# Optimization experiments

Measured on AMD Instinct MI355X. Metric: run time of the kernel, lower is better.

Reference implementation:

```python
import jax, jax.numpy as jnp
import numpy as np

N, E = 20000, 320000
IN, OUT, MID, EC, L = 128, 128, 32, 32, 1
SQRT3 = 1.7320508075688772
EPS = 1e-5


def _xavier(key, fan_in, fan_out, shape=None):
    shape = shape if shape is not None else (fan_in, fan_out)
    std = (2.0 / (fan_in + fan_out)) ** 0.5
    return jax.random.normal(key, shape, dtype=jnp.float32) * std


def layer_norm(x, w, b):
    mu = x.mean(axis=-1, keepdims=True)
    var = ((x - mu) ** 2).mean(axis=-1, keepdims=True)
    return (x - mu) * jax.lax.rsqrt(var + EPS) * w + b


def equ_layer_norm(x, w, b, lmax):
    # x: [N, (lmax+1)^2, C]; per-l RMS norm over (m, channel); l=0 mean-centered + bias.
    segs = []
    for l in range(lmax + 1):
        f = x[:, l * l:(l + 1) * (l + 1), :]
        if l == 0:
            f = f - f.mean(axis=-1, keepdims=True)
        norm = jnp.mean(f * f, axis=(1, 2), keepdims=True)
        f = f * jax.lax.rsqrt(norm + EPS) * w[l]
        if l == 0:
            f = f + b
        segs.append(f)
    return jnp.concatenate(segs, axis=1)


def gate_3j(x, w, lmax, channel):
    # x: [N, (lmax+1)^2, C]; w: [C, C*(lmax+1)] (jax in,out layout)
    after = x[:, 0, :] @ w
    type0 = after[:, :channel]
    mult = jax.nn.sigmoid(after[:, channel:])  # [N, lmax*C]
    parts = [jax.nn.silu(type0)[:, None, :]]
    for l in range(1, lmax + 1):
        parts.append(x[:, l * l:(l + 1) * (l + 1), :] * mult[:, None, (l - 1) * channel:l * channel])
    return jnp.concatenate(parts, axis=1)


def setup_inputs() -> dict:
    key = jax.random.key(0)
    ks = jax.random.split(key, 24)
    inp = {
        'feats': jax.random.normal(ks[0], (N, IN), dtype=jnp.float32),
        'equ': jax.random.normal(ks[1], (N, (L + 1) ** 2, EC), dtype=jnp.float32),
        'points': jax.random.normal(ks[2], (N, 3), dtype=jnp.float32),
        'neighbors': jax.random.randint(ks[3], (2, E), 0, N, dtype=jnp.int64) if jax.config.jax_enable_x64 else jax.random.randint(ks[3], (2, E), 0, N, dtype=jnp.int32),
        # params (jax Linear layout: [in, out])
        'ln1_w': jnp.ones((IN,), jnp.float32), 'ln1_b': jnp.zeros((IN,), jnp.float32),
        'eqn1_w': jnp.ones((L + 1, EC), jnp.float32), 'eqn1_b': jnp.zeros((EC,), jnp.float32),
        'inv_fc_w': _xavier(ks[4], IN, MID), 'inv_fc_b': jnp.zeros((MID,), jnp.float32),
        'equ_fc_w': _xavier(ks[5], EC, MID),
        'fc_l0_w': _xavier(ks[6], 2 * MID, MID), 'fc_l0_b': jnp.zeros((MID,), jnp.float32),
        'equ_fc_2_w': _xavier(ks[7], MID, EC),
        'inv_fc_1_w': _xavier(ks[8], 3 * MID, OUT), 'inv_fc_1_b': jnp.zeros((OUT,), jnp.float32),
        'ffn_ln_w': jnp.ones((OUT,), jnp.float32), 'ffn_ln_b': jnp.zeros((OUT,), jnp.float32),
        'ffn_w1': _xavier(ks[9], OUT, OUT), 'ffn_b1': jnp.zeros((OUT,), jnp.float32),
        'ffn_w2': _xavier(ks[10], OUT, OUT), 'ffn_b2': jnp.zeros((OUT,), jnp.float32),
        'eqn2_w': jnp.ones((L + 1, EC), jnp.float32), 'eqn2_b': jnp.zeros((EC,), jnp.float32),
        'fe1_w': _xavier(ks[11], EC, MID),
        'gate_w': _xavier(ks[12], MID, MID * (L + 1)),
        'fe2_w': _xavier(ks[13], MID, EC),
    }
    return inp


def reference(feats, equ, points, neighbors, ln1_w, ln1_b, eqn1_w, eqn1_b,
              inv_fc_w, inv_fc_b, equ_fc_w, fc_l0_w, fc_l0_b, equ_fc_2_w,
              inv_fc_1_w, inv_fc_1_b, ffn_ln_w, ffn_ln_b, ffn_w1, ffn_b1,
              ffn_w2, ffn_b2, eqn2_w, eqn2_b, fe1_w, gate_w, fe2_w):
    n = feats.shape[0]
    feats = layer_norm(feats, ln1_w, ln1_b)
    equ = equ_layer_norm(equ, eqn1_w, eqn1_b, L)
    feats1 = feats @ inv_fc_w + inv_fc_b              # [N, MID]
    equ1 = equ @ equ_fc_w                              # [N, 4, MID]
    src, dst = neighbors[0], neighbors[1]
    s_equ, t_equ = equ1[src], equ1[dst]                # [E, 4, MID]
    s_feats, t_feats = feats1[src], feats1[dst]        # [E, MID]
    vec = points[src] - points[dst]                    # [E, 3]
    # e3nn spherical harmonics l=0..1, normalize=False, 'component': [1, sqrt(3)*v]
    sh = jnp.concatenate([jnp.ones((vec.shape[0], 1), vec.dtype), SQRT3 * vec], axis=1)  # [E, 4]
    dot1 = jnp.sum(s_equ * t_equ, axis=1)              # [E, MID]
    dot2 = jnp.sum(s_equ * sh[:, :, None], axis=1)     # [E, MID]
    equ_l0 = jax.nn.silu(jnp.concatenate([dot1, dot2], axis=1) @ fc_l0_w + fc_l0_b)
    equ_message = jnp.concatenate([equ_l0[:, None, :], s_equ[:, 1:, :]], axis=1)  # [E, 4, MID]
    equ_message = equ_message @ equ_fc_2_w             # [E, 4, EC]
    inv_message = jax.nn.silu(jnp.concatenate([s_feats, t_feats, equ_l0], axis=-1) @ inv_fc_1_w + inv_fc_1_b)  # [E, OUT]
    nb_cnt = (jnp.max(inv_message, axis=-1, keepdims=True) > 0.0).astype(feats.dtype)  # [E, 1]
    neighbors_new = jnp.ones((n, 1), feats.dtype).at[dst].add(nb_cnt)
    inv_new = jnp.zeros((n, OUT), feats.dtype).at[dst].add(inv_message) + feats  # shortcut1 = Identity
    inv_new = inv_new / neighbors_new
    equ_new = jnp.zeros((n, (L + 1) ** 2, EC), feats.dtype).at[dst].add(equ_message) + equ  # shortcut2 = Identity
    equ_new = equ_new / neighbors_new[:, :, None]
    # ffn_inv
    h = layer_norm(inv_new, ffn_ln_w, ffn_ln_b)
    h = jax.nn.relu(h @ ffn_w1 + ffn_b1) @ ffn_w2 + ffn_b2
    inv_new = h + inv_new
    # ffn_equ
    g = equ_layer_norm(equ_new, eqn2_w, eqn2_b, L) @ fe1_w
    g = gate_3j(g, gate_w, L, MID) @ fe2_w
    equ_new = g + equ_new
    return inv_new, equ_new
```

## Files before the change

kernel.cpp:

```cpp
#include <hip/hip_runtime.h>
#include <math.h>

#define EPS 1e-5f
#define SQRT3F 1.7320508075688772f

__device__ __forceinline__ float wsum64(float x) {
#pragma unroll
    for (int o = 32; o > 0; o >>= 1) x += __shfl_xor(x, o, 64);
    return x;
}
__device__ __forceinline__ float hsum32(float x) {
#pragma unroll
    for (int o = 16; o > 0; o >>= 1) x += __shfl_xor(x, o, 64);
    return x;
}
__device__ __forceinline__ float sigm(float x) { return 1.f / (1.f + __expf(-x)); }
__device__ __forceinline__ float siluf(float x) { return x * sigm(x); }

__global__ __launch_bounds__(256) void node_pre(
    int N,
    const float* __restrict__ feats, const float* __restrict__ equ,
    const float* __restrict__ ln1_w, const float* __restrict__ ln1_b,
    const float* __restrict__ eqn1_w, const float* __restrict__ eqn1_b,
    const float* __restrict__ inv_fc_w, const float* __restrict__ inv_fc_b,
    const float* __restrict__ equ_fc_w, const float* __restrict__ Winv,
    float* __restrict__ feats_ln, float* __restrict__ equ_ln,
    float* __restrict__ equ1t, float* __restrict__ PsP, float* __restrict__ PtP)
{
    __shared__ float fl_s[4][128];
    __shared__ float el_s[4][128];
    __shared__ float f1_s[4][32];
    const int w = threadIdx.x >> 6;
    const int lane = threadIdx.x & 63;
    const int n = blockIdx.x * 4 + w;
    const bool act = n < N;
    const int c = lane & 31;
    const int half = lane >> 5;

    float x0 = 0.f, x1 = 0.f;
    if (act) { x0 = feats[n * 128 + lane]; x1 = feats[n * 128 + 64 + lane]; }
    float s  = wsum64(x0 + x1);
    float sq = wsum64(x0 * x0 + x1 * x1);
    float mu = s * (1.f / 128.f);
    float var = sq * (1.f / 128.f) - mu * mu;
    float rs = rsqrtf(var + EPS);
    float y0 = (x0 - mu) * rs * ln1_w[lane] + ln1_b[lane];
    float y1 = (x1 - mu) * rs * ln1_w[64 + lane] + ln1_b[64 + lane];
    if (act) { feats_ln[n * 128 + lane] = y0; feats_ln[n * 128 + 64 + lane] = y1; }
    fl_s[w][lane] = y0; fl_s[w][64 + lane] = y1;

    float a = 0.f, b = 0.f;
    if (act) { a = equ[n * 128 + lane]; b = equ[n * 128 + 64 + lane]; }
    float a0 = (half == 0) ? a : 0.f;
    float m0 = wsum64(a0) * (1.f / 32.f);
    float f0 = a0 - m0;
    float n0 = wsum64((half == 0) ? f0 * f0 : 0.f) * (1.f / 32.f);
    float rs0 = rsqrtf(n0 + EPS);
    float sq1 = ((half == 1) ? a * a : 0.f) + b * b;
    float n1 = wsum64(sq1) * (1.f / 96.f);
    float rs1 = rsqrtf(n1 + EPS);
    float w1c = eqn1_w[32 + c];
    float ea = (half == 0) ? (f0 * rs0 * eqn1_w[c] + eqn1_b[c]) : (a * rs1 * w1c);
    float eb = b * rs1 * w1c;
    if (act) { equ_ln[n * 128 + lane] = ea; equ_ln[n * 128 + 64 + lane] = eb; }
    el_s[w][lane] = ea; el_s[w][64 + lane] = eb;

    __syncthreads();

    {
        float acc = 0.f;
#pragma unroll 8
        for (int k = 0; k < 64; k++) {
            int kk = half * 64 + k;
            acc += fl_s[w][kk] * inv_fc_w[kk * 32 + c];
        }
        acc += __shfl_xor(acc, 32);
        if (half == 0) f1_s[w][c] = acc + inv_fc_b[c];
    }
    if (act) {
        float acc = 0.f, acc2 = 0.f;
#pragma unroll 8
        for (int k = 0; k < 32; k++) {
            float wv = equ_fc_w[k * 32 + c];
            acc  += el_s[w][half * 32 + k] * wv;
            acc2 += el_s[w][(half + 2) * 32 + k] * wv;
        }
        equ1t[n * 128 + c * 4 + half]     = acc;
        equ1t[n * 128 + c * 4 + half + 2] = acc2;
    }
    __syncthreads();
    if (!act) return;

    {
        const int jj = c;
        float4 aPs = {0.f, 0.f, 0.f, 0.f};
        float4 aPt = {0.f, 0.f, 0.f, 0.f};
#pragma unroll 4
        for (int k = 0; k < 16; k++) {
            int kk = half * 16 + k;
            float x = f1_s[w][kk];
            float4 w4 = *(const float4*)&Winv[kk * 128 + jj * 4];
            float4 v4 = *(const float4*)&Winv[(32 + kk) * 128 + jj * 4];
            aPs.x += x * w4.x; aPs.y += x * w4.y; aPs.z += x * w4.z; aPs.w += x * w4.w;
            aPt.x += x * v4.x; aPt.y += x * v4.y; aPt.z += x * v4.z; aPt.w += x * v4.w;
        }
        aPs.x += __shfl_xor(aPs.x, 32); aPs.y += __shfl_xor(aPs.y, 32);
        aPs.z += __shfl_xor(aPs.z, 32); aPs.w += __shfl_xor(aPs.w, 32);
        aPt.x += __shfl_xor(aPt.x, 32); aPt.y += __shfl_xor(aPt.y, 32);
        aPt.z += __shfl_xor(aPt.z, 32); aPt.w += __shfl_xor(aPt.w, 32);
        if (half == 0) {
            const float* ps = (const float*)&aPs;
            const float* pt = (const float*)&aPt;
#pragma unroll
            for (int i = 0; i < 4; i++) {
                int m = jj * 4 + i;
                PsP[n * 128 + (m & 31) * 4 + (m >> 5)] = ps[i];
                PtP[n * 128 + (m & 31) * 4 + (m >> 5)] = pt[i];
            }
        }
    }
}

__global__ __launch_bounds__(256) void csr_hist(int E, const int* __restrict__ nb,
                                                int* __restrict__ deg)
{
    int i = blockIdx.x * 256 + threadIdx.x;
    if (i < E) atomicAdd(&deg[nb[E + i]], 1);
}

__global__ __launch_bounds__(1024) void csr_scan(int N, const int* __restrict__ deg,
                                                 int* __restrict__ row_start,
                                                 int* __restrict__ cursor)
{
    __shared__ int part[1024];
    const int t = threadIdx.x;
    const int per = (N + 1023) / 1024;
    const int base = t * per;
    int s = 0;
    for (int i = 0; i < per; i++) { int idx = base + i; if (idx < N) s += deg[idx]; }
    part[t] = s;
    __syncthreads();
    for (int off = 1; off < 1024; off <<= 1) {
        int v = (t >= off) ? part[t - off] : 0;
        __syncthreads();
        part[t] += v;
        __syncthreads();
    }
    int run = (t > 0) ? part[t - 1] : 0;
    for (int i = 0; i < per; i++) {
        int idx = base + i;
        if (idx < N) { row_start[idx] = run; cursor[idx] = run; run += deg[idx]; }
    }
}

__global__ __launch_bounds__(256) void csr_scatter(int E, const int* __restrict__ nb,
                                                   int* __restrict__ cursor,
                                                   int* __restrict__ csr_src)
{
    int i = blockIdx.x * 256 + threadIdx.x;
    if (i < E) {
        int d = nb[E + i];
        int s = nb[i];
        int pos = atomicAdd(&cursor[d], 1);
        csr_src[pos] = s;
    }
}

__global__ __launch_bounds__(256) void edge_agg(
    int N,
    const int* __restrict__ row_start, const int* __restrict__ deg_arr,
    const int* __restrict__ csr_src,
    const float* __restrict__ points, const float* __restrict__ equ1t,
    const float* __restrict__ PsP, const float* __restrict__ PtP,
    const float* __restrict__ feats_ln, const float* __restrict__ equ_ln,
    const float* __restrict__ Wl0g, const float* __restrict__ bl0g,
    const float* __restrict__ We2g, const float* __restrict__ Winvg,
    const float* __restrict__ binvg,
    float* __restrict__ out_inv, float* __restrict__ out_equ)
{
    __shared__ float WeP[32 * 128];
    __shared__ float Wl0P[16 * 128];
    __shared__ float We2P[8 * 128];
    __shared__ float BinvP[128];
    __shared__ float bl0s[32];
    __shared__ float scr[8][128];

    for (int idx = threadIdx.x; idx < 4096; idx += 256) {
        int k = idx >> 7, r = idx & 127, cc = r >> 2, j = r & 3;
        WeP[idx] = Winvg[(64 + k) * 128 + j * 32 + cc];
    }
    for (int idx = threadIdx.x; idx < 2048; idx += 256) {
        int g = idx >> 7, r = idx & 127, cc = r >> 2, i = r & 3;
        Wl0P[idx] = Wl0g[(g * 4 + i) * 32 + cc];
    }
    for (int idx = threadIdx.x; idx < 1024; idx += 256) {
        int g = idx >> 7, r = idx & 127, cc = r >> 2, i = r & 3;
        We2P[idx] = We2g[(g * 4 + i) * 32 + cc];
    }
    if (threadIdx.x < 128) BinvP[threadIdx.x] = binvg[(threadIdx.x & 3) * 32 + (threadIdx.x >> 2)];
    if (threadIdx.x < 32) bl0s[threadIdx.x] = bl0g[threadIdx.x];
    __syncthreads();

    const int grp = threadIdx.x >> 5;
    const int c = threadIdx.x & 31;
    const int halfsel = grp & 1;
    const int n = blockIdx.x * 8 + grp;
    if (n >= N) return;

    const int start = row_start[n];
    const int len = deg_arr[n];
    float4 te4 = *(const float4*)&equ1t[n * 128 + c * 4];
    float4 pt4 = *(const float4*)&PtP[n * 128 + c * 4];
    const float pdx = points[n * 3 + 0], pdy = points[n * 3 + 1], pdz = points[n * 3 + 2];
    float4 base = *(const float4*)&BinvP[c * 4];
    base.x += pt4.x; base.y += pt4.y; base.z += pt4.z; base.w += pt4.w;

    float4 acc = {0.f, 0.f, 0.f, 0.f};
    float4 aer = {0.f, 0.f, 0.f, 0.f};
    int cnt = 0;
    int i = 0;

    for (; i + 2 <= len; i += 2) {
        const int s0 = csr_src[start + i];
        const int s1 = csr_src[start + i + 1];
        float4 a0 = *(const float4*)&equ1t[s0 * 128 + c * 4];
        float4 a1 = *(const float4*)&equ1t[s1 * 128 + c * 4];
        float4 p0 = *(const float4*)&PsP[s0 * 128 + c * 4];
        float4 p1 = *(const float4*)&PsP[s1 * 128 + c * 4];
        float dx0 = SQRT3F * (points[s0 * 3 + 0] - pdx);
        float dy0 = SQRT3F * (points[s0 * 3 + 1] - pdy);
        float dz0 = SQRT3F * (points[s0 * 3 + 2] - pdz);
        float dx1 = SQRT3F * (points[s1 * 3 + 0] - pdx);
        float dy1 = SQRT3F * (points[s1 * 3 + 1] - pdy);
        float dz1 = SQRT3F * (points[s1 * 3 + 2] - pdz);
        scr[grp][c]      = a0.x * te4.x + a0.y * te4.y + a0.z * te4.z + a0.w * te4.w;
        scr[grp][32 + c] = a0.x + a0.y * dx0 + a0.z * dy0 + a0.w * dz0;
        scr[grp][64 + c] = a1.x * te4.x + a1.y * te4.y + a1.z * te4.z + a1.w * te4.w;
        scr[grp][96 + c] = a1.x + a1.y * dx1 + a1.z * dy1 + a1.w * dz1;

        float e0acc = bl0s[c], e1acc = bl0s[c];
#pragma unroll
        for (int g = 0; g < 16; g++) {
            float4 w4 = *(const float4*)&Wl0P[g * 128 + c * 4];
            float4 d0 = *(const float4*)&scr[grp][g * 4];
            float4 d1 = *(const float4*)&scr[grp][64 + g * 4];
            e0acc += d0.x * w4.x + d0.y * w4.y + d0.z * w4.z + d0.w * w4.w;
            e1acc += d1.x * w4.x + d1.y * w4.y + d1.z * w4.z + d1.w * w4.w;
        }
        float el0_0 = siluf(e0acc);
        float el0_1 = siluf(e1acc);
        aer.x += el0_0 + el0_1;
        aer.y += a0.y + a1.y; aer.z += a0.z + a1.z; aer.w += a0.w + a1.w;
        scr[grp][c] = el0_0;
        scr[grp][32 + c] = el0_1;

        float4 m0 = base, m1 = base;
        m0.x += p0.x; m0.y += p0.y; m0.z += p0.z; m0.w += p0.w;
        m1.x += p1.x; m1.y += p1.y; m1.z += p1.z; m1.w += p1.w;
#pragma unroll
        for (int g = 0; g < 8; g++) {
            float4 x0 = *(const float4*)&scr[grp][g * 4];
            float4 x1 = *(const float4*)&scr[grp][32 + g * 4];
            const float* xp0 = (const float*)&x0;
            const float* xp1 = (const float*)&x1;
#pragma unroll
            for (int t = 0; t < 4; t++) {
                float4 w4 = *(const float4*)&WeP[(g * 4 + t) * 128 + c * 4];
                float v0 = xp0[t], v1 = xp1[t];
                m0.x += v0 * w4.x; m0.y += v0 * w4.y; m0.z += v0 * w4.z; m0.w += v0 * w4.w;
                m1.x += v1 * w4.x; m1.y += v1 * w4.y; m1.z += v1 * w4.z; m1.w += v1 * w4.w;
            }
        }
        m0.x = siluf(m0.x); m0.y = siluf(m0.y); m0.z = siluf(m0.z); m0.w = siluf(m0.w);
        m1.x = siluf(m1.x); m1.y = siluf(m1.y); m1.z = siluf(m1.z); m1.w = siluf(m1.w);
        acc.x += m0.x + m1.x; acc.y += m0.y + m1.y;
        acc.z += m0.z + m1.z; acc.w += m0.w + m1.w;
        float mx0 = fmaxf(fmaxf(m0.x, m0.y), fmaxf(m0.z, m0.w));
        float mx1 = fmaxf(fmaxf(m1.x, m1.y), fmaxf(m1.z, m1.w));
        unsigned long long b0 = __ballot(mx0 > 0.f);
        unsigned long long b1 = __ballot(mx1 > 0.f);
        cnt += ((unsigned int)(b0 >> (halfsel * 32)) != 0u);
        cnt += ((unsigned int)(b1 >> (halfsel * 32)) != 0u);
    }
    for (; i < len; i++) {
        const int s0 = csr_src[start + i];
        float4 a0 = *(const float4*)&equ1t[s0 * 128 + c * 4];
        float4 p0 = *(const float4*)&PsP[s0 * 128 + c * 4];
        float dx0 = SQRT3F * (points[s0 * 3 + 0] - pdx);
        float dy0 = SQRT3F * (points[s0 * 3 + 1] - pdy);
        float dz0 = SQRT3F * (points[s0 * 3 + 2] - pdz);
        scr[grp][c]      = a0.x * te4.x + a0.y * te4.y + a0.z * te4.z + a0.w * te4.w;
        scr[grp][32 + c] = a0.x + a0.y * dx0 + a0.z * dy0 + a0.w * dz0;
        float e0acc = bl0s[c];
#pragma unroll
        for (int g = 0; g < 16; g++) {
            float4 w4 = *(const float4*)&Wl0P[g * 128 + c * 4];
            float4 d0 = *(const float4*)&scr[grp][g * 4];
            e0acc += d0.x * w4.x + d0.y * w4.y + d0.z * w4.z + d0.w * w4.w;
        }
        float el0_0 = siluf(e0acc);
        aer.x += el0_0; aer.y += a0.y; aer.z += a0.z; aer.w += a0.w;
        scr[grp][c] = el0_0;
        float4 m0 = base;
        m0.x += p0.x; m0.y += p0.y; m0.z += p0.z; m0.w += p0.w;
#pragma unroll
        for (int g = 0; g < 8; g++) {
            float4 x0 = *(const float4*)&scr[grp][g * 4];
            const float* xp0 = (const float*)&x0;
#pragma unroll
            for (int t = 0; t < 4; t++) {
                float4 w4 = *(const float4*)&WeP[(g * 4 + t) * 128 + c * 4];
                float v0 = xp0[t];
                m0.x += v0 * w4.x; m0.y += v0 * w4.y; m0.z += v0 * w4.z; m0.w += v0 * w4.w;
            }
        }
        m0.x = siluf(m0.x); m0.y = siluf(m0.y); m0.z = siluf(m0.z); m0.w = siluf(m0.w);
        acc.x += m0.x; acc.y += m0.y; acc.z += m0.z; acc.w += m0.w;
        float mx0 = fmaxf(fmaxf(m0.x, m0.y), fmaxf(m0.z, m0.w));
        unsigned long long b0 = __ballot(mx0 > 0.f);
        cnt += ((unsigned int)(b0 >> (halfsel * 32)) != 0u);
    }

    const float inv_nbn = 1.f / (1.f + (float)cnt);
    out_inv[n * 128 + c]      = (acc.x + feats_ln[n * 128 + c])      * inv_nbn;
    out_inv[n * 128 + 32 + c] = (acc.y + feats_ln[n * 128 + 32 + c]) * inv_nbn;
    out_inv[n * 128 + 64 + c] = (acc.z + feats_ln[n * 128 + 64 + c]) * inv_nbn;
    out_inv[n * 128 + 96 + c] = (acc.w + feats_ln[n * 128 + 96 + c]) * inv_nbn;

    *(float4*)&scr[grp][c * 4] = aer;
    float4 eo = {0.f, 0.f, 0.f, 0.f};
#pragma unroll
    for (int g = 0; g < 8; g++) {
        float4 w4 = *(const float4*)&We2P[g * 128 + c * 4];
        const float* wp = (const float*)&w4;
#pragma unroll
        for (int t = 0; t < 4; t++) {
            float4 a4 = *(const float4*)&scr[grp][(g * 4 + t) * 4];
            float wv = wp[t];
            eo.x += a4.x * wv; eo.y += a4.y * wv; eo.z += a4.z * wv; eo.w += a4.w * wv;
        }
    }
    out_equ[n * 128 + c]      = (eo.x + equ_ln[n * 128 + c])      * inv_nbn;
    out_equ[n * 128 + 32 + c] = (eo.y + equ_ln[n * 128 + 32 + c]) * inv_nbn;
    out_equ[n * 128 + 64 + c] = (eo.z + equ_ln[n * 128 + 64 + c]) * inv_nbn;
    out_equ[n * 128 + 96 + c] = (eo.w + equ_ln[n * 128 + 96 + c]) * inv_nbn;
}

__global__ __launch_bounds__(256) void node_post(
    int N,
    const float* __restrict__ ffn_ln_w, const float* __restrict__ ffn_ln_b,
    const float* __restrict__ W1g, const float* __restrict__ b1g,
    const float* __restrict__ W2g, const float* __restrict__ b2g,
    const float* __restrict__ eqn2_w, const float* __restrict__ eqn2_b,
    const float* __restrict__ fe1, const float* __restrict__ gate_w,
    const float* __restrict__ fe2,
    float* __restrict__ io_inv, float* __restrict__ io_equ)
{
    __shared__ float ht[128 * 36];
    __shared__ float es[8][128];
    __shared__ float gs[8][128];
    __shared__ float fe1P[8 * 128];
    __shared__ float fe2P[8 * 128];
    __shared__ float gatePa[8 * 128];
    __shared__ float gatePb[8 * 128];

    for (int idx = threadIdx.x; idx < 1024; idx += 256) {
        int g = idx >> 7, r = idx & 127, cc = r >> 2, i = r & 3;
        fe1P[idx]   = fe1[(g * 4 + i) * 32 + cc];
        fe2P[idx]   = fe2[(g * 4 + i) * 32 + cc];
        gatePa[idx] = gate_w[(g * 4 + i) * 64 + cc];
        gatePb[idx] = gate_w[(g * 4 + i) * 64 + 32 + cc];
    }
    __syncthreads();

    const int grp = threadIdx.x >> 5;
    const int c = threadIdx.x & 31;

    for (int q = 0; q < 4; q++) {
        const int nd = grp * 4 + q;
        const int n = blockIdx.x * 32 + nd;
        if (n >= N) break;

        float eq0 = io_equ[n * 128 + c];
        float eq1 = io_equ[n * 128 + 32 + c];
        float eq2 = io_equ[n * 128 + 64 + c];
        float eq3 = io_equ[n * 128 + 96 + c];
        float m0 = hsum32(eq0) * (1.f / 32.f);
        float f0 = eq0 - m0;
        float n0 = hsum32(f0 * f0) * (1.f / 32.f);
        float rs0 = rsqrtf(n0 + EPS);
        float n1 = hsum32(eq1 * eq1 + eq2 * eq2 + eq3 * eq3) * (1.f / 96.f);
        float rs1 = rsqrtf(n1 + EPS);
        float w1c = eqn2_w[32 + c];
        float4 ev;
        ev.x = f0 * rs0 * eqn2_w[c] + eqn2_b[c];
        ev.y = eq1 * rs1 * w1c;
        ev.z = eq2 * rs1 * w1c;
        ev.w = eq3 * rs1 * w1c;
        *(float4*)&es[grp][c * 4] = ev;

        float4 g4 = {0.f, 0.f, 0.f, 0.f};
#pragma unroll
        for (int g = 0; g < 8; g++) {
            float4 w4 = *(const float4*)&fe1P[g * 128 + c * 4];
            const float* wp = (const float*)&w4;
#pragma unroll
            for (int t = 0; t < 4; t++) {
                float4 a4 = *(const float4*)&es[grp][(g * 4 + t) * 4];
                float wv = wp[t];
                g4.x += a4.x * wv; g4.y += a4.y * wv; g4.z += a4.z * wv; g4.w += a4.w * wv;
            }
        }
        *(float4*)&gs[grp][c * 4] = g4;

        float aftA = 0.f, aftB = 0.f;
#pragma unroll
        for (int g = 0; g < 8; g++) {
            float4 wa4 = *(const float4*)&gatePa[g * 128 + c * 4];
            float4 wb4 = *(const float4*)&gatePb[g * 128 + c * 4];
            const float* wap = (const float*)&wa4;
            const float* wbp = (const float*)&wb4;
#pragma unroll
            for (int t = 0; t < 4; t++) {
                float g0 = gs[grp][(g * 4 + t) * 4];
                aftA += g0 * wap[t];
                aftB += g0 * wbp[t];
            }
        }
        float mult = sigm(aftB);
        float4 G;
        G.x = siluf(aftA);
        G.y = g4.y * mult; G.z = g4.z * mult; G.w = g4.w * mult;
        *(float4*)&es[grp][c * 4] = G;

        float4 oo = {0.f, 0.f, 0.f, 0.f};
#pragma unroll
        for (int g = 0; g < 8; g++) {
            float4 w4 = *(const float4*)&fe2P[g * 128 + c * 4];
            const float* wp = (const float*)&w4;
#pragma unroll
            for (int t = 0; t < 4; t++) {
                float4 a4 = *(const float4*)&es[grp][(g * 4 + t) * 4];
                float wv = wp[t];
                oo.x += a4.x * wv; oo.y += a4.y * wv; oo.z += a4.z * wv; oo.w += a4.w * wv;
            }
        }
        io_equ[n * 128 + c]      = oo.x + eq0;
        io_equ[n * 128 + 32 + c] = oo.y + eq1;
        io_equ[n * 128 + 64 + c] = oo.z + eq2;
        io_equ[n * 128 + 96 + c] = oo.w + eq3;

        float ip0 = io_inv[n * 128 + c];
        float ip1 = io_inv[n * 128 + 32 + c];
        float ip2 = io_inv[n * 128 + 64 + c];
        float ip3 = io_inv[n * 128 + 96 + c];
        float sm = hsum32(ip0 + ip1 + ip2 + ip3) * (1.f / 128.f);
        float sv = hsum32(ip0 * ip0 + ip1 * ip1 + ip2 * ip2 + ip3 * ip3) * (1.f / 128.f) - sm * sm;
        float rsv = rsqrtf(sv + EPS);
        ht[c * 36 + nd]         = (ip0 - sm) * rsv * ffn_ln_w[c]      + ffn_ln_b[c];
        ht[(32 + c) * 36 + nd]  = (ip1 - sm) * rsv * ffn_ln_w[32 + c] + ffn_ln_b[32 + c];
        ht[(64 + c) * 36 + nd]  = (ip2 - sm) * rsv * ffn_ln_w[64 + c] + ffn_ln_b[64 + c];
        ht[(96 + c) * 36 + nd]  = (ip3 - sm) * rsv * ffn_ln_w[96 + c] + ffn_ln_b[96 + c];
    }

    const int wid = threadIdx.x >> 6;
    const int half = (threadIdx.x >> 5) & 1;
    const int ndbase = wid * 8;
    const int nbase = blockIdx.x * 32 + ndbase;

    float4 acc8[8];
#pragma unroll
    for (int j = 0; j < 8; j++) acc8[j] = make_float4(0.f, 0.f, 0.f, 0.f);
    for (int k = 0; k < 64; k++) {
        const int kk = half * 64 + k;
        float4 w4 = *(const float4*)&W1g[kk * 128 + c * 4];
        float4 xA = *(const float4*)&ht[kk * 36 + ndbase];
        float4 xB = *(const float4*)&ht[kk * 36 + ndbase + 4];
        const float* xa = (const float*)&xA;
        const float* xb = (const float*)&xB;
#pragma unroll
        for (int j = 0; j < 4; j++) {
            float v = xa[j];
            acc8[j].x += v * w4.x; acc8[j].y += v * w4.y; acc8[j].z += v * w4.z; acc8[j].w += v * w4.w;
            float u = xb[j];
            acc8[4 + j].x += u * w4.x; acc8[4 + j].y += u * w4.y; acc8[4 + j].z += u * w4.z; acc8[4 + j].w += u * w4.w;
        }
    }
#pragma unroll
    for (int j = 0; j < 8; j++) {
        acc8[j].x += __shfl_xor(acc8[j].x, 32); acc8[j].y += __shfl_xor(acc8[j].y, 32);
        acc8[j].z += __shfl_xor(acc8[j].z, 32); acc8[j].w += __shfl_xor(acc8[j].w, 32);
    }
    if (half == 0) {
        float4 b4 = *(const float4*)&b1g[c * 4];
#pragma unroll
        for (int j = 0; j < 8; j++) {
            float r0 = fmaxf(acc8[j].x + b4.x, 0.f);
            float r1 = fmaxf(acc8[j].y + b4.y, 0.f);
            float r2 = fmaxf(acc8[j].z + b4.z, 0.f);
            float r3 = fmaxf(acc8[j].w + b4.w, 0.f);
            ht[(4 * c + 0) * 36 + ndbase + j] = r0;
            ht[(4 * c + 1) * 36 + ndbase + j] = r1;
            ht[(4 * c + 2) * 36 + ndbase + j] = r2;
            ht[(4 * c + 3) * 36 + ndbase + j] = r3;
        }
    }
#pragma unroll
    for (int j = 0; j < 8; j++) acc8[j] = make_float4(0.f, 0.f, 0.f, 0.f);
    for (int k = 0; k < 64; k++) {
        const int kk = half * 64 + k;
        float4 w4 = *(const float4*)&W2g[kk * 128 + c * 4];
        float4 xA = *(const float4*)&ht[kk * 36 + ndbase];
        float4 xB = *(const float4*)&ht[kk * 36 + ndbase + 4];
        const float* xa = (const float*)&xA;
        const float* xb = (const float*)&xB;
#pragma unroll
        for (int j = 0; j < 4; j++) {
            float v = xa[j];
            acc8[j].x += v * w4.x; acc8[j].y += v * w4.y; acc8[j].z += v * w4.z; acc8[j].w += v * w4.w;
            float u = xb[j];
            acc8[4 + j].x += u * w4.x; acc8[4 + j].y += u * w4.y; acc8[4 + j].z += u * w4.z; acc8[4 + j].w += u * w4.w;
        }
    }
#pragma unroll
    for (int j = 0; j < 8; j++) {
        acc8[j].x += __shfl_xor(acc8[j].x, 32); acc8[j].y += __shfl_xor(acc8[j].y, 32);
        acc8[j].z += __shfl_xor(acc8[j].z, 32); acc8[j].w += __shfl_xor(acc8[j].w, 32);
    }
    if (half == 0) {
        float4 b4 = *(const float4*)&b2g[c * 4];
#pragma unroll
        for (int j = 0; j < 8; j++) {
            const int n = nbase + j;
            if (n < N) {
                float4 ipre = *(const float4*)&io_inv[n * 128 + c * 4];
                float4 o;
                o.x = acc8[j].x + b4.x + ipre.x;
                o.y = acc8[j].y + b4.y + ipre.y;
                o.z = acc8[j].z + b4.z + ipre.z;
                o.w = acc8[j].w + b4.w + ipre.w;
                *(float4*)&io_inv[n * 128 + c * 4] = o;
            }
        }
    }
}

extern "C" void kernel_launch(void* const* d_in, const int* in_sizes, int n_in,
                              void* d_out, int out_size, void* d_ws, size_t ws_size,
                              hipStream_t stream)
{
    const float* feats     = (const float*)d_in[0];
    const float* equ       = (const float*)d_in[1];
    const float* points    = (const float*)d_in[2];
    const int*   neighbors = (const int*)d_in[3];
    const float* ln1_w     = (const float*)d_in[4];
    const float* ln1_b     = (const float*)d_in[5];
    const float* eqn1_w    = (const float*)d_in[6];
    const float* eqn1_b    = (const float*)d_in[7];
    const float* inv_fc_w  = (const float*)d_in[8];
    const float* inv_fc_b  = (const float*)d_in[9];
    const float* equ_fc_w  = (const float*)d_in[10];
    const float* fc_l0_w   = (const float*)d_in[11];
    const float* fc_l0_b   = (const float*)d_in[12];
    const float* equ_fc_2_w= (const float*)d_in[13];
    const float* inv_fc_1_w= (const float*)d_in[14];
    const float* inv_fc_1_b= (const float*)d_in[15];
    const float* ffn_ln_w  = (const float*)d_in[16];
    const float* ffn_ln_b  = (const float*)d_in[17];
    const float* ffn_w1    = (const float*)d_in[18];
    const float* ffn_b1    = (const float*)d_in[19];
    const float* ffn_w2    = (const float*)d_in[20];
    const float* ffn_b2    = (const float*)d_in[21];
    const float* eqn2_w    = (const float*)d_in[22];
    const float* eqn2_b    = (const float*)d_in[23];
    const float* fe1_w     = (const float*)d_in[24];
    const float* gate_w    = (const float*)d_in[25];
    const float* fe2_w     = (const float*)d_in[26];

    const int N = in_sizes[0] / 128;
    const int E = in_sizes[3] / 2;

    float* ws = (float*)d_ws;
    float* feats_ln = ws;
    float* equ_ln   = feats_ln + (size_t)N * 128;
    float* equ1t    = equ_ln   + (size_t)N * 128;
    float* PsP      = equ1t    + (size_t)N * 128;
    float* PtP      = PsP      + (size_t)N * 128;
    int* deg        = (int*)(PtP + (size_t)N * 128);
    int* row_start  = deg + N;
    int* cursor     = row_start + N;
    int* csr_src    = cursor + N;

    hipMemsetAsync(deg, 0, (size_t)N * sizeof(int), stream);

    node_pre<<<(N + 3) / 4, 256, 0, stream>>>(
        N, feats, equ, ln1_w, ln1_b, eqn1_w, eqn1_b,
        inv_fc_w, inv_fc_b, equ_fc_w, inv_fc_1_w,
        feats_ln, equ_ln, equ1t, PsP, PtP);

    csr_hist<<<(E + 255) / 256, 256, 0, stream>>>(E, neighbors, deg);
    csr_scan<<<1, 1024, 0, stream>>>(N, deg, row_start, cursor);
    csr_scatter<<<(E + 255) / 256, 256, 0, stream>>>(E, neighbors, cursor, csr_src);

    float* out_inv = (float*)d_out;
    float* out_equ = out_inv + (size_t)N * 128;

    edge_agg<<<(N + 7) / 8, 256, 0, stream>>>(
        N, row_start, deg, csr_src,
        points, equ1t, PsP, PtP, feats_ln, equ_ln,
        fc_l0_w, fc_l0_b, equ_fc_2_w, inv_fc_1_w, inv_fc_1_b,
        out_inv, out_equ);

    node_post<<<(N + 31) / 32, 256, 0, stream>>>(
        N, ffn_ln_w, ffn_ln_b, ffn_w1, ffn_b1, ffn_w2, ffn_b2,
        eqn2_w, eqn2_b, fe1_w, gate_w, fe2_w,
        out_inv, out_equ);
}
```

Before: 512.5 us.

## Restructure edge aggregation with persistent blocks, split-wave edges, and 4-edge batching

The edge aggregation kernel moves from one 32-lane group per node to one 64-lane wave per node. The two half-waves each take half of the node's edges, process them in batches of 4 so every weight load from shared memory is reused across four edges, and combine their partial sums with cross-half shuffles. The grid becomes a fixed persistent grid of 1280 blocks that loops over node chunks, which amortizes the per-block shared-weight staging across many nodes. The CSR degree histogram is folded into the node preprocessing launch as extra blocks to save one kernel launch. The cost is padded work on tail batches (clamped indices plus masking) and higher register pressure from the 4-edge batches.

```diff
diff --git a/kernel.cpp b/kernel.cpp
--- a/kernel.cpp
+++ b/kernel.cpp
@@ -17,16 +17,24 @@
 __device__ __forceinline__ float sigm(float x) { return 1.f / (1.f + __expf(-x)); }
 __device__ __forceinline__ float siluf(float x) { return x * sigm(x); }
 
-__global__ __launch_bounds__(256) void node_pre(
-    int N,
+__global__ __launch_bounds__(256) void pre_and_hist(
+    int N, int E, int nb_pre,
     const float* __restrict__ feats, const float* __restrict__ equ,
+    const int* __restrict__ nbrs,
     const float* __restrict__ ln1_w, const float* __restrict__ ln1_b,
     const float* __restrict__ eqn1_w, const float* __restrict__ eqn1_b,
     const float* __restrict__ inv_fc_w, const float* __restrict__ inv_fc_b,
     const float* __restrict__ equ_fc_w, const float* __restrict__ Winv,
     float* __restrict__ feats_ln, float* __restrict__ equ_ln,
-    float* __restrict__ equ1t, float* __restrict__ PsP, float* __restrict__ PtP)
+    float* __restrict__ equ1t, float* __restrict__ PsP, float* __restrict__ PtP,
+    int* __restrict__ deg)
 {
+    if (blockIdx.x >= nb_pre) {
+        int i = (blockIdx.x - nb_pre) * 256 + threadIdx.x;
+        if (i < E) atomicAdd(&deg[nbrs[E + i]], 1);
+        return;
+    }
+
     __shared__ float fl_s[4][128];
     __shared__ float el_s[4][128];
     __shared__ float f1_s[4][32];
@@ -119,13 +127,6 @@
             }
         }
     }
-}
-
-__global__ __launch_bounds__(256) void csr_hist(int E, const int* __restrict__ nb,
-                                                int* __restrict__ deg)
-{
-    int i = blockIdx.x * 256 + threadIdx.x;
-    if (i < E) atomicAdd(&deg[nb[E + i]], 1);
 }
 
 __global__ __launch_bounds__(1024) void csr_scan(int N, const int* __restrict__ deg,
@@ -183,7 +184,7 @@
     __shared__ float We2P[8 * 128];
     __shared__ float BinvP[128];
     __shared__ float bl0s[32];
-    __shared__ float scr[8][128];
+    __shared__ float scr[4][512];
 
     for (int idx = threadIdx.x; idx < 4096; idx += 256) {
         int k = idx >> 7, r = idx & 127, cc = r >> 2, j = r & 3;
@@ -201,149 +202,141 @@
     if (threadIdx.x < 32) bl0s[threadIdx.x] = bl0g[threadIdx.x];
     __syncthreads();
 
-    const int grp = threadIdx.x >> 5;
-    const int c = threadIdx.x & 31;
-    const int halfsel = grp & 1;
-    const int n = blockIdx.x * 8 + grp;
-    if (n >= N) return;
-
-    const int start = row_start[n];
-    const int len = deg_arr[n];
-    float4 te4 = *(const float4*)&equ1t[n * 128 + c * 4];
-    float4 pt4 = *(const float4*)&PtP[n * 128 + c * 4];
-    const float pdx = points[n * 3 + 0], pdy = points[n * 3 + 1], pdz = points[n * 3 + 2];
-    float4 base = *(const float4*)&BinvP[c * 4];
-    base.x += pt4.x; base.y += pt4.y; base.z += pt4.z; base.w += pt4.w;
-
-    float4 acc = {0.f, 0.f, 0.f, 0.f};
-    float4 aer = {0.f, 0.f, 0.f, 0.f};
-    int cnt = 0;
-    int i = 0;
-
-    for (; i + 2 <= len; i += 2) {
-        const int s0 = csr_src[start + i];
-        const int s1 = csr_src[start + i + 1];
-        float4 a0 = *(const float4*)&equ1t[s0 * 128 + c * 4];
-        float4 a1 = *(const float4*)&equ1t[s1 * 128 + c * 4];
-        float4 p0 = *(const float4*)&PsP[s0 * 128 + c * 4];
-        float4 p1 = *(const float4*)&PsP[s1 * 128 + c * 4];
-        float dx0 = SQRT3F * (points[s0 * 3 + 0] - pdx);
-        float dy0 = SQRT3F * (points[s0 * 3 + 1] - pdy);
-        float dz0 = SQRT3F * (points[s0 * 3 + 2] - pdz);
-        float dx1 = SQRT3F * (points[s1 * 3 + 0] - pdx);
-        float dy1 = SQRT3F * (points[s1 * 3 + 1] - pdy);
-        float dz1 = SQRT3F * (points[s1 * 3 + 2] - pdz);
-        scr[grp][c]      = a0.x * te4.x + a0.y * te4.y + a0.z * te4.z + a0.w * te4.w;
-        scr[grp][32 + c] = a0.x + a0.y * dx0 + a0.z * dy0 + a0.w * dz0;
-        scr[grp][64 + c] = a1.x * te4.x + a1.y * te4.y + a1.z * te4.z + a1.w * te4.w;
-        scr[grp][96 + c] = a1.x + a1.y * dx1 + a1.z * dy1 + a1.w * dz1;
-
-        float e0acc = bl0s[c], e1acc = bl0s[c];
-#pragma unroll
-        for (int g = 0; g < 16; g++) {
-            float4 w4 = *(const float4*)&Wl0P[g * 128 + c * 4];
-            float4 d0 = *(const float4*)&scr[grp][g * 4];
-            float4 d1 = *(const float4*)&scr[grp][64 + g * 4];
-            e0acc += d0.x * w4.x + d0.y * w4.y + d0.z * w4.z + d0.w * w4.w;
-            e1acc += d1.x * w4.x + d1.y * w4.y + d1.z * w4.z + d1.w * w4.w;
-        }
-        float el0_0 = siluf(e0acc);
-        float el0_1 = siluf(e1acc);
-        aer.x += el0_0 + el0_1;
-        aer.y += a0.y + a1.y; aer.z += a0.z + a1.z; aer.w += a0.w + a1.w;
-        scr[grp][c] = el0_0;
-        scr[grp][32 + c] = el0_1;
-
-        float4 m0 = base, m1 = base;
-        m0.x += p0.x; m0.y += p0.y; m0.z += p0.z; m0.w += p0.w;
-        m1.x += p1.x; m1.y += p1.y; m1.z += p1.z; m1.w += p1.w;
-#pragma unroll
-        for (int g = 0; g < 8; g++) {
-            float4 x0 = *(const float4*)&scr[grp][g * 4];
-            float4 x1 = *(const float4*)&scr[grp][32 + g * 4];
-            const float* xp0 = (const float*)&x0;
-            const float* xp1 = (const float*)&x1;
-#pragma unroll
-            for (int t = 0; t < 4; t++) {
-                float4 w4 = *(const float4*)&WeP[(g * 4 + t) * 128 + c * 4];
-                float v0 = xp0[t], v1 = xp1[t];
-                m0.x += v0 * w4.x; m0.y += v0 * w4.y; m0.z += v0 * w4.z; m0.w += v0 * w4.w;
-                m1.x += v1 * w4.x; m1.y += v1 * w4.y; m1.z += v1 * w4.z; m1.w += v1 * w4.w;
-            }
-        }
-        m0.x = siluf(m0.x); m0.y = siluf(m0.y); m0.z = siluf(m0.z); m0.w = siluf(m0.w);
-        m1.x = siluf(m1.x); m1.y = siluf(m1.y); m1.z = siluf(m1.z); m1.w = siluf(m1.w);
-        acc.x += m0.x + m1.x; acc.y += m0.y + m1.y;
-        acc.z += m0.z + m1.z; acc.w += m0.w + m1.w;
-        float mx0 = fmaxf(fmaxf(m0.x, m0.y), fmaxf(m0.z, m0.w));
-        float mx1 = fmaxf(fmaxf(m1.x, m1.y), fmaxf(m1.z, m1.w));
-        unsigned long long b0 = __ballot(mx0 > 0.f);
-        unsigned long long b1 = __ballot(mx1 > 0.f);
-        cnt += ((unsigned int)(b0 >> (halfsel * 32)) != 0u);
-        cnt += ((unsigned int)(b1 >> (halfsel * 32)) != 0u);
-    }
-    for (; i < len; i++) {
-        const int s0 = csr_src[start + i];
-        float4 a0 = *(const float4*)&equ1t[s0 * 128 + c * 4];
-        float4 p0 = *(const float4*)&PsP[s0 * 128 + c * 4];
-        float dx0 = SQRT3F * (points[s0 * 3 + 0] - pdx);
-        float dy0 = SQRT3F * (points[s0 * 3 + 1] - pdy);
-        float dz0 = SQRT3F * (points[s0 * 3 + 2] - pdz);
-        scr[grp][c]      = a0.x * te4.x + a0.y * te4.y + a0.z * te4.z + a0.w * te4.w;
-        scr[grp][32 + c] = a0.x + a0.y * dx0 + a0.z * dy0 + a0.w * dz0;
-        float e0acc = bl0s[c];
-#pragma unroll
-        for (int g = 0; g < 16; g++) {
-            float4 w4 = *(const float4*)&Wl0P[g * 128 + c * 4];
-            float4 d0 = *(const float4*)&scr[grp][g * 4];
-            e0acc += d0.x * w4.x + d0.y * w4.y + d0.z * w4.z + d0.w * w4.w;
-        }
-        float el0_0 = siluf(e0acc);
-        aer.x += el0_0; aer.y += a0.y; aer.z += a0.z; aer.w += a0.w;
-        scr[grp][c] = el0_0;
-        float4 m0 = base;
-        m0.x += p0.x; m0.y += p0.y; m0.z += p0.z; m0.w += p0.w;
-#pragma unroll
-        for (int g = 0; g < 8; g++) {
-            float4 x0 = *(const float4*)&scr[grp][g * 4];
-            const float* xp0 = (const float*)&x0;
-#pragma unroll
-            for (int t = 0; t < 4; t++) {
-                float4 w4 = *(const float4*)&WeP[(g * 4 + t) * 128 + c * 4];
-                float v0 = xp0[t];
-                m0.x += v0 * w4.x; m0.y += v0 * w4.y; m0.z += v0 * w4.z; m0.w += v0 * w4.w;
-            }
-        }
-        m0.x = siluf(m0.x); m0.y = siluf(m0.y); m0.z = siluf(m0.z); m0.w = siluf(m0.w);
-        acc.x += m0.x; acc.y += m0.y; acc.z += m0.z; acc.w += m0.w;
-        float mx0 = fmaxf(fmaxf(m0.x, m0.y), fmaxf(m0.z, m0.w));
-        unsigned long long b0 = __ballot(mx0 > 0.f);
-        cnt += ((unsigned int)(b0 >> (halfsel * 32)) != 0u);
-    }
-
-    const float inv_nbn = 1.f / (1.f + (float)cnt);
-    out_inv[n * 128 + c]      = (acc.x + feats_ln[n * 128 + c])      * inv_nbn;
-    out_inv[n * 128 + 32 + c] = (acc.y + feats_ln[n * 128 + 32 + c]) * inv_nbn;
-    out_inv[n * 128 + 64 + c] = (acc.z + feats_ln[n * 128 + 64 + c]) * inv_nbn;
-    out_inv[n * 128 + 96 + c] = (acc.w + feats_ln[n * 128 + 96 + c]) * inv_nbn;
-
-    *(float4*)&scr[grp][c * 4] = aer;
-    float4 eo = {0.f, 0.f, 0.f, 0.f};
-#pragma unroll
-    for (int g = 0; g < 8; g++) {
-        float4 w4 = *(const float4*)&We2P[g * 128 + c * 4];
-        const float* wp = (const float*)&w4;
-#pragma unroll
-        for (int t = 0; t < 4; t++) {
-            float4 a4 = *(const float4*)&scr[grp][(g * 4 + t) * 4];
-            float wv = wp[t];
-            eo.x += a4.x * wv; eo.y += a4.y * wv; eo.z += a4.z * wv; eo.w += a4.w * wv;
-        }
-    }
-    out_equ[n * 128 + c]      = (eo.x + equ_ln[n * 128 + c])      * inv_nbn;
-    out_equ[n * 128 + 32 + c] = (eo.y + equ_ln[n * 128 + 32 + c]) * inv_nbn;
-    out_equ[n * 128 + 64 + c] = (eo.z + equ_ln[n * 128 + 64 + c]) * inv_nbn;
-    out_equ[n * 128 + 96 + c] = (eo.w + equ_ln[n * 128 + 96 + c]) * inv_nbn;
+    const int w = threadIdx.x >> 6;
+    const int lane = threadIdx.x & 63;
+    const int h = lane >> 5;
+    const int c = lane & 31;
+    float* sc = &scr[w][h * 256];
+
+    const int nchunk = (N + 3) / 4;
+    for (int chunk = blockIdx.x; chunk < nchunk; chunk += gridDim.x) {
+        const int n = chunk * 4 + w;
+        if (n >= N) continue;
+
+        const int start = row_start[n];
+        const int len = deg_arr[n];
+        const int nh0 = (len + 1) >> 1;
+        const int hstart = start + (h ? nh0 : 0);
+        const int hlen = h ? (len - nh0) : nh0;
+
+        float4 te4 = *(const float4*)&equ1t[n * 128 + c * 4];
+        float4 pt4 = *(const float4*)&PtP[n * 128 + c * 4];
+        const float pdx = points[n * 3 + 0];
+        const float pdy = points[n * 3 + 1];
+        const float pdz = points[n * 3 + 2];
+        float4 base = *(const float4*)&BinvP[c * 4];
+        base.x += pt4.x; base.y += pt4.y; base.z += pt4.z; base.w += pt4.w;
+
+        float4 acc = {0.f, 0.f, 0.f, 0.f};
+        float4 aer = {0.f, 0.f, 0.f, 0.f};
+        int cnt = 0;
+
+        for (int i = 0; i < hlen; i += 4) {
+            const int v = hlen - i;
+            int s[4];
+#pragma unroll
+            for (int t = 0; t < 4; t++) {
+                int ii = i + t; if (ii > hlen - 1) ii = hlen - 1;
+                s[t] = csr_src[hstart + ii];
+            }
+            float4 p[4];
+            float e[4];
+#pragma unroll
+            for (int t = 0; t < 4; t++) {
+                float4 a4 = *(const float4*)&equ1t[s[t] * 128 + c * 4];
+                p[t] = *(const float4*)&PsP[s[t] * 128 + c * 4];
+                float dx = SQRT3F * (points[s[t] * 3 + 0] - pdx);
+                float dy = SQRT3F * (points[s[t] * 3 + 1] - pdy);
+                float dz = SQRT3F * (points[s[t] * 3 + 2] - pdz);
+                sc[t * 64 + c]      = a4.x * te4.x + a4.y * te4.y + a4.z * te4.z + a4.w * te4.w;
+                sc[t * 64 + 32 + c] = a4.x + a4.y * dx + a4.z * dy + a4.w * dz;
+                if (t < v) { aer.y += a4.y; aer.z += a4.z; aer.w += a4.w; }
+            }
+#pragma unroll
+            for (int t = 0; t < 4; t++) e[t] = bl0s[c];
+#pragma unroll
+            for (int g = 0; g < 16; g++) {
+                float4 w4 = *(const float4*)&Wl0P[g * 128 + c * 4];
+#pragma unroll
+                for (int t = 0; t < 4; t++) {
+                    float4 d4 = *(const float4*)&sc[t * 64 + g * 4];
+                    e[t] += d4.x * w4.x + d4.y * w4.y + d4.z * w4.z + d4.w * w4.w;
+                }
+            }
+#pragma unroll
+            for (int t = 0; t < 4; t++) {
+                e[t] = siluf(e[t]);
+                sc[t * 64 + c] = e[t];
+                if (t < v) aer.x += e[t];
+            }
+            float4 m[4];
+#pragma unroll
+            for (int t = 0; t < 4; t++) {
+                m[t] = base;
+                m[t].x += p[t].x; m[t].y += p[t].y; m[t].z += p[t].z; m[t].w += p[t].w;
+            }
+#pragma unroll
+            for (int g = 0; g < 8; g++) {
+                float4 x4[4];
+#pragma unroll
+                for (int t = 0; t < 4; t++) x4[t] = *(const float4*)&sc[t * 64 + g * 4];
+#pragma unroll
+                for (int u = 0; u < 4; u++) {
+                    float4 w4 = *(const float4*)&WeP[(g * 4 + u) * 128 + c * 4];
+#pragma unroll
+                    for (int t = 0; t < 4; t++) {
+                        float x = ((const float*)&x4[t])[u];
+                        m[t].x += x * w4.x; m[t].y += x * w4.y;
+                        m[t].z += x * w4.z; m[t].w += x * w4.w;
+                    }
+                }
+            }
+#pragma unroll
+            for (int t = 0; t < 4; t++) {
+                float4 mm;
+                mm.x = siluf(m[t].x); mm.y = siluf(m[t].y);
+                mm.z = siluf(m[t].z); mm.w = siluf(m[t].w);
+                float mx = fmaxf(fmaxf(mm.x, mm.y), fmaxf(mm.z, mm.w));
+                unsigned long long bal = __ballot(mx > 0.f);
+                if (t < v) {
+                    acc.x += mm.x; acc.y += mm.y; acc.z += mm.z; acc.w += mm.w;
+                    cnt += ((unsigned int)(bal >> (h * 32)) != 0u);
+                }
+            }
+        }
+
+        acc.x += __shfl_xor(acc.x, 32); acc.y += __shfl_xor(acc.y, 32);
+        acc.z += __shfl_xor(acc.z, 32); acc.w += __shfl_xor(acc.w, 32);
+        aer.x += __shfl_xor(aer.x, 32); aer.y += __shfl_xor(aer.y, 32);
+        aer.z += __shfl_xor(aer.z, 32); aer.w += __shfl_xor(aer.w, 32);
+        cnt += __shfl_xor(cnt, 32);
+
+        const float inv_nbn = 1.f / (1.f + (float)cnt);
+        if (h == 0) {
+            out_inv[n * 128 + c]      = (acc.x + feats_ln[n * 128 + c])      * inv_nbn;
+            out_inv[n * 128 + 32 + c] = (acc.y + feats_ln[n * 128 + 32 + c]) * inv_nbn;
+            out_inv[n * 128 + 64 + c] = (acc.z + feats_ln[n * 128 + 64 + c]) * inv_nbn;
+            out_inv[n * 128 + 96 + c] = (acc.w + feats_ln[n * 128 + 96 + c]) * inv_nbn;
+
+            *(float4*)&scr[w][c * 4] = aer;
+            float4 eo = {0.f, 0.f, 0.f, 0.f};
+#pragma unroll
+            for (int g = 0; g < 8; g++) {
+                float4 w4 = *(const float4*)&We2P[g * 128 + c * 4];
+                const float* wp = (const float*)&w4;
+#pragma unroll
+                for (int t = 0; t < 4; t++) {
+                    float4 a4 = *(const float4*)&scr[w][(g * 4 + t) * 4];
+                    float wv = wp[t];
+                    eo.x += a4.x * wv; eo.y += a4.y * wv; eo.z += a4.z * wv; eo.w += a4.w * wv;
+                }
+            }
+            out_equ[n * 128 + c]      = (eo.x + equ_ln[n * 128 + c])      * inv_nbn;
+            out_equ[n * 128 + 32 + c] = (eo.y + equ_ln[n * 128 + 32 + c]) * inv_nbn;
+            out_equ[n * 128 + 64 + c] = (eo.z + equ_ln[n * 128 + 64 + c]) * inv_nbn;
+            out_equ[n * 128 + 96 + c] = (eo.w + equ_ln[n * 128 + 96 + c]) * inv_nbn;
+        }
+    }
 }
 
 __global__ __launch_bounds__(256) void node_post(
@@ -495,14 +488,10 @@
         float4 b4 = *(const float4*)&b1g[c * 4];
 #pragma unroll
         for (int j = 0; j < 8; j++) {
-            float r0 = fmaxf(acc8[j].x + b4.x, 0.f);
-            float r1 = fmaxf(acc8[j].y + b4.y, 0.f);
-            float r2 = fmaxf(acc8[j].z + b4.z, 0.f);
-            float r3 = fmaxf(acc8[j].w + b4.w, 0.f);
-            ht[(4 * c + 0) * 36 + ndbase + j] = r0;
-            ht[(4 * c + 1) * 36 + ndbase + j] = r1;
-            ht[(4 * c + 2) * 36 + ndbase + j] = r2;
-            ht[(4 * c + 3) * 36 + ndbase + j] = r3;
+            ht[(4 * c + 0) * 36 + ndbase + j] = fmaxf(acc8[j].x + b4.x, 0.f);
+            ht[(4 * c + 1) * 36 + ndbase + j] = fmaxf(acc8[j].y + b4.y, 0.f);
+            ht[(4 * c + 2) * 36 + ndbase + j] = fmaxf(acc8[j].z + b4.z, 0.f);
+            ht[(4 * c + 3) * 36 + ndbase + j] = fmaxf(acc8[j].w + b4.w, 0.f);
         }
     }
 #pragma unroll
@@ -593,19 +582,21 @@
 
     hipMemsetAsync(deg, 0, (size_t)N * sizeof(int), stream);
 
-    node_pre<<<(N + 3) / 4, 256, 0, stream>>>(
-        N, feats, equ, ln1_w, ln1_b, eqn1_w, eqn1_b,
+    const int nb_pre = (N + 3) / 4;
+    const int nb_hist = (E + 255) / 256;
+    pre_and_hist<<<nb_pre + nb_hist, 256, 0, stream>>>(
+        N, E, nb_pre, feats, equ, neighbors,
+        ln1_w, ln1_b, eqn1_w, eqn1_b,
         inv_fc_w, inv_fc_b, equ_fc_w, inv_fc_1_w,
-        feats_ln, equ_ln, equ1t, PsP, PtP);
-
-    csr_hist<<<(E + 255) / 256, 256, 0, stream>>>(E, neighbors, deg);
+        feats_ln, equ_ln, equ1t, PsP, PtP, deg);
+
     csr_scan<<<1, 1024, 0, stream>>>(N, deg, row_start, cursor);
     csr_scatter<<<(E + 255) / 256, 256, 0, stream>>>(E, neighbors, cursor, csr_src);
 
     float* out_inv = (float*)d_out;
     float* out_equ = out_inv + (size_t)N * 128;
 
-    edge_agg<<<(N + 7) / 8, 256, 0, stream>>>(
+    edge_agg<<<1280, 256, 0, stream>>>(
         N, row_start, deg, csr_src,
         points, equ1t, PsP, PtP, feats_ln, equ_ln,
         fc_l0_w, fc_l0_b, equ_fc_2_w, inv_fc_1_w, inv_fc_1_b,
```

Result: slower. 547.2 us (+6.8%).
